# Kernel optimization log

Measured on AMD Instinct MI355X. Metric: run time of the kernel, lower is better.

The kernel has to match this reference:

```python
import jax, jax.numpy as jnp
import numpy as np
from jax import lax

B, C, H, W = 2, 3, 1024, 1024
SH, SW = 128, 128
FH, FW = H // SH, W // SW  # integer pooling factors (8, 8)
NPRE = 64
L = 0.24          # diffusion step size l
K = 0.03          # exp(log(0.03)), fixed logk for feature_extractor='none'
EPS = 1e-8
DEPS = 0.1


def _g(x):
    # g(x) = 1 / (1 + |x*x| / K^2)
    return 1.0 / (1.0 + (x * x) / (K * K))


def _conductance(feats):
    # cv: [B,1,H-1,W], ch: [B,1,H,W-1]; mean of |finite diff| over channels
    cv = _g(jnp.mean(jnp.abs(feats[:, :, 1:, :] - feats[:, :, :-1, :]), axis=1, keepdims=True))
    ch = _g(jnp.mean(jnp.abs(feats[:, :, :, 1:] - feats[:, :, :, :-1]), axis=1, keepdims=True))
    return cv, ch


def _downsample(x):
    # AdaptiveAvgPool2d((SH,SW)) with integer factor == exact mean pooling
    b = x.shape[0]
    return x.reshape(b, 1, SH, FH, SW, FW).mean(axis=(3, 5))


def _upsample(x):
    # F.interpolate(mode='nearest') with integer factor == pixel replication
    return jnp.repeat(jnp.repeat(x, FH, axis=2), FW, axis=3)


def setup_inputs() -> dict:
    key = jax.random.key(0)
    k1, k2, k3, k4 = jax.random.split(key, 4)
    guide = jax.random.normal(k1, (B, C, H, W), dtype=jnp.float32)
    y_bicubic = jax.random.uniform(k2, (B, 1, H, W), dtype=jnp.float32)
    source = jax.random.uniform(k3, (B, 1, SH, SW), dtype=jnp.float32)
    mask_lr = jax.random.uniform(k4, (B, 1, SH, SW), dtype=jnp.float32)
    return {"guide": guide, "y_bicubic": y_bicubic, "source": source, "mask_lr": mask_lr}


def _diffuse(img, guide, source, mask_inv):
    # feature_extractor == 'none': guide_feats = cat([guide, img], 1)
    feats = jnp.concatenate([guide, img], axis=1)
    cv, ch = _conductance(feats)

    def step(im, _):
        # diffuse_step: dv/dh computed from the SAME input image, then
        # vertical update applied first, horizontal second (matches torch in-place order)
        dv = im[:, :, 1:, :] - im[:, :, :-1, :]
        dh = im[:, :, :, 1:] - im[:, :, :, :-1]
        tv = L * cv * dv
        th = L * ch * dh
        im = im.at[:, :, 1:, :].add(-tv).at[:, :, :-1, :].add(tv)
        im = im.at[:, :, :, 1:].add(-th).at[:, :, :, :-1].add(th)
        # adjust_step: low-res ratio correction
        im_ss = _downsample(im)
        ratio_ss = jnp.where(mask_inv, 1.0, source / (im_ss + EPS))
        return im * _upsample(ratio_ss), None

    img, _ = lax.scan(step, img, None, length=NPRE)
    return img, cv, ch


def reference(guide, y_bicubic, source, mask_lr):
    # shift depths if min(source) <= deps (jit-safe scalar select)
    shift = jnp.where(jnp.min(source) <= DEPS, DEPS, 0.0).astype(source.dtype)
    source = source + shift
    img = y_bicubic + shift
    mask_inv = mask_lr < 0.5
    y_pred, cv, ch = _diffuse(img, guide, source, mask_inv)
    y_pred = y_pred - shift
    return y_pred, cv, ch
```

## Files before the change

kernel.cpp:

```cpp
#include <hip/hip_runtime.h>


#define BB 2
#define HH 1024
#define WW 1024
#define NPIX (HH * WW)
#define CVN (1023 * 1024)
#define SHW (128 * 128)
#define LL 0.24f
#define KK2 (0.03f * 0.03f)
#define EPSF 1e-8f
#define DEPSF 0.1f
#define NPRE 64
#define NB 512
#define TPB 256

typedef unsigned long long u64;
typedef unsigned int uint4v __attribute__((ext_vector_type(4)));
#define ROWPAR ((size_t)NB * 2 * 128)
#define COLPAR ((size_t)NB * 2 * 32)

__device__ inline void ust4(void* p, uint4v q) {
    asm volatile("global_store_dwordx4 %0, %1, off sc0 sc1" :: "v"(p), "v"(q) : "memory");
}
__device__ inline uint4v uld4(const void* p) {
    uint4v r;
    asm volatile("global_load_dwordx4 %0, %1, off sc0 sc1" : "=v"(r) : "v"(p) : "memory");
    return r;
}
__device__ inline void vwait() { asm volatile("s_waitcnt vmcnt(0)" ::: "memory"); }

__device__ inline void pub2(u64* p, float v0, float v1, unsigned s) {
    uint4v q;
    q.x = __float_as_uint(v0); q.y = s;
    q.z = __float_as_uint(v1); q.w = s;
    ust4(p, q);
}
__device__ inline bool tags_ok(uint4v a, uint4v b, unsigned s) {
    return a.y == s && a.w == s && b.y == s && b.w == s;
}
__device__ inline float4 vals_of(uint4v a, uint4v b) {
    return make_float4(__uint_as_float(a.x), __uint_as_float(a.z),
                       __uint_as_float(b.x), __uint_as_float(b.z));
}

__device__ inline float gfun(float d) { return 1.0f / (1.0f + (d * d) / KK2); }

#define BAR() do { asm volatile("s_waitcnt lgkmcnt(0)" ::: "memory"); \
                   __builtin_amdgcn_s_barrier();                      \
                   __builtin_amdgcn_sched_barrier(0); } while (0)

__launch_bounds__(TPB, 2)
__global__ void persist_kernel(const float* __restrict__ guide, const float* __restrict__ yb,
                               const float* __restrict__ src, const float* __restrict__ mask,
                               float* __restrict__ out, float* __restrict__ out_cv,
                               float* __restrict__ out_ch,
                               u64* __restrict__ bufRow, u64* __restrict__ bufCol) {
    __shared__ float tile[2][32 * 128];
    __shared__ float sm[4];
    int blk = blockIdx.x;
    int b = blk >> 8;
    int r = blk & 255;
    int tileY = r >> 3;
    int tileX = r & 7;
    int tid = threadIdx.x;
    int cyL = tid >> 5;
    int g = tid & 31;
    int wv = tid >> 6;
    int l0 = tid & 63;
    int lx0 = g * 4;
    int ly0 = cyL * 4;
    int gx = tileX * 128 + lx0;
    int gy = tileY * 32 + ly0;

    float mmin = 1e30f;
    const float4* s4 = (const float4*)src;
    for (int i = tid; i < (BB * SHW) / 4; i += TPB) {
        float4 v = s4[i];
        mmin = fminf(mmin, fminf(fminf(v.x, v.y), fminf(v.z, v.w)));
    }
    for (int off = 32; off > 0; off >>= 1) mmin = fminf(mmin, __shfl_down(mmin, off));
    if ((tid & 63) == 0) sm[tid >> 6] = mmin;
    __syncthreads();
    float mm = fminf(fminf(sm[0], sm[1]), fminf(sm[2], sm[3]));
    float shift = (mm <= DEPSF) ? DEPSF : 0.0f;

    int ry[6];
#pragma unroll
    for (int j = 0; j < 6; ++j) {
        int y = gy - 1 + j;
        ry[j] = y < 0 ? 0 : (y > 1023 ? 1023 : y);
    }
    int cxl = (gx > 0) ? gx - 1 : 0;
    int cxr = (gx + 4 < 1024) ? gx + 4 : 1023;
    float4 z4 = make_float4(0.f, 0.f, 0.f, 0.f);
    float4 vd[5] = {z4, z4, z4, z4, z4};
    float4 hd[4] = {z4, z4, z4, z4};
    float hmd[4] = {0.f, 0.f, 0.f, 0.f};
    float4 imv[4], r0v = z4, r5v = z4;
    float slv[4], srv[4];
#pragma unroll
    for (int c = 0; c < 4; ++c) {
        const float* F = (c < 3) ? guide + ((size_t)b * 3 + c) * NPIX
                                 : yb + (size_t)b * NPIX;
        float4 rr[6];
#pragma unroll
        for (int j = 0; j < 6; ++j)
            rr[j] = *(const float4*)(F + (size_t)ry[j] * WW + gx);
#pragma unroll
        for (int j = 0; j < 5; ++j) {
            vd[j].x += fabsf(rr[j + 1].x - rr[j].x);
            vd[j].y += fabsf(rr[j + 1].y - rr[j].y);
            vd[j].z += fabsf(rr[j + 1].z - rr[j].z);
            vd[j].w += fabsf(rr[j + 1].w - rr[j].w);
        }
#pragma unroll
        for (int k = 0; k < 4; ++k) {
            float4 R = rr[k + 1];
            float sr = F[(size_t)ry[k + 1] * WW + cxr];
            float sl = F[(size_t)ry[k + 1] * WW + cxl];
            hd[k].x += fabsf(R.y - R.x);
            hd[k].y += fabsf(R.z - R.y);
            hd[k].z += fabsf(R.w - R.z);
            hd[k].w += fabsf(sr - R.w);
            hmd[k] += fabsf(R.x - sl);
            if (c == 3) { imv[k] = R; slv[k] = sl; srv[k] = sr; }
        }
        if (c == 3) { r0v = rr[0]; r5v = rr[5]; }
    }
    float4 cvR[5], chR[4];
    float hmR[4];
#pragma unroll
    for (int j = 0; j < 5; ++j) {
        int y = gy - 1 + j;
        if (y < 0 || y > 1022) {
            cvR[j] = z4;
        } else {
            cvR[j] = make_float4(gfun(vd[j].x * 0.25f), gfun(vd[j].y * 0.25f),
                                 gfun(vd[j].z * 0.25f), gfun(vd[j].w * 0.25f));
        }
    }
#pragma unroll
    for (int k = 0; k < 4; ++k) {
        chR[k] = make_float4(gfun(hd[k].x * 0.25f), gfun(hd[k].y * 0.25f),
                             gfun(hd[k].z * 0.25f), gfun(hd[k].w * 0.25f));
        if (gx + 3 == 1023) chR[k].w = 0.f;
        hmR[k] = (gx > 0) ? gfun(hmd[k] * 0.25f) : 0.f;
    }
#pragma unroll
    for (int j = 1; j < 5; ++j) {
        int y = gy + j - 1;
        if (y <= 1022)
            *(float4*)(out_cv + (size_t)b * CVN + (size_t)y * WW + gx) = cvR[j];
    }
#pragma unroll
    for (int k = 0; k < 4; ++k) {
        float* base = out_ch + (size_t)b * CVN + (size_t)(gy + k) * 1023;
        base[gx + 0] = chR[k].x;
        base[gx + 1] = chR[k].y;
        base[gx + 2] = chR[k].z;
        if (gx + 3 < 1023) base[gx + 3] = chR[k].w;
    }

    int sidx = b * SHW + (tileY * 4 + (cyL >> 1)) * 128 + tileX * 16 + (g >> 1);
    float sval = src[sidx] + shift;
    bool masked = mask[sidx] < 0.5f;

    bool upAct = (cyL == 0 && tileY > 0);
    bool dnAct = (cyL == 7 && tileY < 31);
    bool lAct  = (g == 0  && tileX > 0);
    bool rAct  = (g == 31 && tileX < 7);
    bool pubTop = (wv == 0 && tileY > 0);
    bool pubBot = (wv == 3 && tileY < 31);

    float* cur = &tile[0][0];
    float* nxt = &tile[1][0];

#pragma unroll
    for (int k = 0; k < 4; ++k) {
        float4 v = imv[k];
        v.x += shift; v.y += shift; v.z += shift; v.w += shift;
        *(float4*)&cur[(ly0 + k) * 128 + lx0] = v;
    }
    float4 hUp = z4, hDn = z4;
    float xlR[4] = {0.f, 0.f, 0.f, 0.f}, xrR[4] = {0.f, 0.f, 0.f, 0.f};
    if (upAct) { hUp = r0v; hUp.x += shift; hUp.y += shift; hUp.z += shift; hUp.w += shift; }
    if (dnAct) { hDn = r5v; hDn.x += shift; hDn.y += shift; hDn.z += shift; hDn.w += shift; }
    if (lAct) {
#pragma unroll
        for (int k = 0; k < 4; ++k) xlR[k] = slv[k] + shift;
    }
    if (rAct) {
#pragma unroll
        for (int k = 0; k < 4; ++k) xrR[k] = srv[k] + shift;
    }
    __syncthreads();

    float4 nv[4];
    for (int t = 0; t < NPRE; ++t) {
        float4 rUp = (cyL == 0) ? hUp : *(float4*)&cur[(ly0 - 1) * 128 + lx0];
        float4 rC  = *(float4*)&cur[ly0 * 128 + lx0];
        float csum = 0.f;
#pragma unroll
        for (int k = 0; k < 4; ++k) {
            float4 rDn = (k == 3 && cyL == 7) ? hDn
                       : *(float4*)&cur[(ly0 + 1 + k) * 128 + lx0];
            float4 cu = cvR[k], cd = cvR[k + 1], h4 = chR[k];
            float xl = __shfl_up(rC.w, 1);
            float xr = __shfl_down(rC.x, 1);
            float hm = hmR[k];
            if (g == 0)  xl = xlR[k];
            if (g == 31) xr = xrR[k];
            float4 a;
            a.x = rC.x + LL * (cd.x * (rDn.x - rC.x) - cu.x * (rC.x - rUp.x)
                             + h4.x * (rC.y - rC.x) - hm   * (rC.x - xl));
            a.y = rC.y + LL * (cd.y * (rDn.y - rC.y) - cu.y * (rC.y - rUp.y)
                             + h4.y * (rC.z - rC.y) - h4.x * (rC.y - rC.x));
            a.z = rC.z + LL * (cd.z * (rDn.z - rC.z) - cu.z * (rC.z - rUp.z)
                             + h4.z * (rC.w - rC.z) - h4.y * (rC.z - rC.y));
            a.w = rC.w + LL * (cd.w * (rDn.w - rC.w) - cu.w * (rC.w - rUp.w)
                             + h4.w * (xr   - rC.w) - h4.z * (rC.w - rC.z));
            nv[k] = a;
            csum += a.x + a.y + a.z + a.w;
            rUp = rC; rC = rDn;
        }
        csum += __shfl_xor(csum, 1);
        csum += __shfl_xor(csum, 32);
        float ratio = masked ? 1.0f : sval / (csum * (1.0f / 64.0f) + EPSF);

        if (t == NPRE - 1) {
            float* ob = out + (size_t)b * NPIX;
#pragma unroll
            for (int k = 0; k < 4; ++k) {
                float4 v = nv[k];
                v.x = v.x * ratio - shift; v.y = v.y * ratio - shift;
                v.z = v.z * ratio - shift; v.w = v.w * ratio - shift;
                *(float4*)(ob + (size_t)(gy + k) * WW + gx) = v;
            }
            break;
        }
#pragma unroll
        for (int k = 0; k < 4; ++k) {
            nv[k].x *= ratio; nv[k].y *= ratio; nv[k].z *= ratio; nv[k].w *= ratio;
        }

        unsigned s2 = (unsigned)(t + 1);
        size_t rOff2 = (s2 & 1) ? ROWPAR : 0;
        size_t cOff2 = (s2 & 1) ? COLPAR : 0;
        if (pubTop) {
            float a = __shfl(nv[0].x, l0 >> 1), bq = __shfl(nv[0].y, l0 >> 1);
            float c = __shfl(nv[0].z, l0 >> 1), d = __shfl(nv[0].w, l0 >> 1);
            float v0 = (l0 & 1) ? c : a, v1 = (l0 & 1) ? d : bq;
            uint4v q; q.x = __float_as_uint(v0); q.y = s2;
            q.z = __float_as_uint(v1); q.w = s2;
            ust4(&bufRow[rOff2 + ((size_t)blk * 2 + 0) * 128 + 2 * l0], q);
        }
        if (pubBot) {
            int sl = 32 + (l0 >> 1);
            float a = __shfl(nv[3].x, sl), bq = __shfl(nv[3].y, sl);
            float c = __shfl(nv[3].z, sl), d = __shfl(nv[3].w, sl);
            float v0 = (l0 & 1) ? c : a, v1 = (l0 & 1) ? d : bq;
            uint4v q; q.x = __float_as_uint(v0); q.y = s2;
            q.z = __float_as_uint(v1); q.w = s2;
            ust4(&bufRow[rOff2 + ((size_t)blk * 2 + 1) * 128 + 2 * l0], q);
        }
        if (lAct) {
            u64* p = &bufCol[cOff2 + ((size_t)blk * 2 + 0) * 32 + ly0];
            pub2(p, nv[0].x, nv[1].x, s2);
            pub2(p + 2, nv[2].x, nv[3].x, s2);
        }
        if (rAct) {
            u64* p = &bufCol[cOff2 + ((size_t)blk * 2 + 1) * 32 + ly0];
            pub2(p, nv[0].w, nv[1].w, s2);
            pub2(p + 2, nv[2].w, nv[3].w, s2);
        }

#pragma unroll
        for (int k = 0; k < 4; ++k)
            *(float4*)&nxt[(ly0 + k) * 128 + lx0] = nv[k];
        BAR();

        const u64* pUp = upAct ? &bufRow[rOff2 + (((size_t)blk - 8) * 2 + 1) * 128 + lx0] : nullptr;
        const u64* pDn = dnAct ? &bufRow[rOff2 + (((size_t)blk + 8) * 2 + 0) * 128 + lx0] : nullptr;
        const u64* pL  = lAct  ? &bufCol[cOff2 + (((size_t)blk - 1) * 2 + 1) * 32 + ly0] : nullptr;
        const u64* pR  = rAct  ? &bufCol[cOff2 + (((size_t)blk + 1) * 2 + 0) * 32 + ly0] : nullptr;
        bool needU = upAct, needD = dnAct, needL = lAct, needR = rAct;
        uint4v uA, uB, dA, dB, lA, lB, rA, rB;
        for (;;) {
            if (needU) { uA = uld4(pUp); uB = uld4(pUp + 2); }
            if (needD) { dA = uld4(pDn); dB = uld4(pDn + 2); }
            if (needL) { lA = uld4(pL);  lB = uld4(pL + 2); }
            if (needR) { rA = uld4(pR);  rB = uld4(pR + 2); }
            vwait();
            if (needU && tags_ok(uA, uB, s2)) { hUp = vals_of(uA, uB); needU = false; }
            if (needD && tags_ok(dA, dB, s2)) { hDn = vals_of(dA, dB); needD = false; }
            if (needL && tags_ok(lA, lB, s2)) {
                float4 c = vals_of(lA, lB);
                xlR[0] = c.x; xlR[1] = c.y; xlR[2] = c.z; xlR[3] = c.w;
                needL = false;
            }
            if (needR && tags_ok(rA, rB, s2)) {
                float4 c = vals_of(rA, rB);
                xrR[0] = c.x; xrR[1] = c.y; xrR[2] = c.z; xrR[3] = c.w;
                needR = false;
            }
            if (__all(!(needU || needD || needL || needR))) break;
            __builtin_amdgcn_s_sleep(1);
        }
        float* tmp = cur; cur = nxt; nxt = tmp;
    }
}

extern "C" void kernel_launch(void* const* d_in, const int* in_sizes, int n_in,
                              void* d_out, int out_size, void* d_ws, size_t ws_size,
                              hipStream_t stream) {
    const float* guide = (const float*)d_in[0];
    const float* yb    = (const float*)d_in[1];
    const float* src   = (const float*)d_in[2];
    const float* mask  = (const float*)d_in[3];

    float* out    = (float*)d_out;
    float* out_cv = out + (size_t)BB * NPIX;
    float* out_ch = out_cv + (size_t)BB * CVN;

    u64* bufRow = (u64*)d_ws;
    u64* bufCol = bufRow + 2 * ROWPAR;

    persist_kernel<<<NB, TPB, 0, stream>>>(guide, yb, src, mask, out, out_cv,
                                           out_ch, bufRow, bufCol);
}
```

Measured before the change: 254.0 us.

## Overlap halo polling with interior stencil compute in persistent diffusion loop

The halo exchange wait moves from the end of each iteration to the start of the next. Halo loads are issued first, then the interior stencil is computed with zero halos, and halo contributions are added as linear corrections once the tagged values arrive. This hides inter-block communication latency behind compute. It adds correction arithmetic and relies on the tag and sequence indexing (sP = t, parity buffers) matching what the publishers wrote.

New measurement: 231.6 us. 8.9% less time.

```diff
diff --git a/kernel.cpp b/kernel.cpp
--- a/kernel.cpp
+++ b/kernel.cpp
@@ -198,19 +198,35 @@
 
     float4 nv[4];
     for (int t = 0; t < NPRE; ++t) {
-        float4 rUp = (cyL == 0) ? hUp : *(float4*)&cur[(ly0 - 1) * 128 + lx0];
+        unsigned sP = (unsigned)t;
+        size_t rOffP = (t & 1) ? ROWPAR : 0;
+        size_t cOffP = (t & 1) ? COLPAR : 0;
+        const u64* pUp = upAct ? &bufRow[rOffP + (((size_t)blk - 8) * 2 + 1) * 128 + lx0] : nullptr;
+        const u64* pDn = dnAct ? &bufRow[rOffP + (((size_t)blk + 8) * 2 + 0) * 128 + lx0] : nullptr;
+        const u64* pL  = lAct  ? &bufCol[cOffP + (((size_t)blk - 1) * 2 + 1) * 32 + ly0] : nullptr;
+        const u64* pR  = rAct  ? &bufCol[cOffP + (((size_t)blk + 1) * 2 + 0) * 32 + ly0] : nullptr;
+        uint4v uA, uB, dA, dB, lA, lB, rA, rB;
+        bool pollRound = (t > 0);
+        if (pollRound) {
+            if (upAct) { uA = uld4(pUp); uB = uld4(pUp + 2); }
+            if (dnAct) { dA = uld4(pDn); dB = uld4(pDn + 2); }
+            if (lAct)  { lA = uld4(pL);  lB = uld4(pL + 2); }
+            if (rAct)  { rA = uld4(pR);  rB = uld4(pR + 2); }
+        }
+
+        float4 rUp = (cyL == 0) ? z4 : *(float4*)&cur[(ly0 - 1) * 128 + lx0];
         float4 rC  = *(float4*)&cur[ly0 * 128 + lx0];
         float csum = 0.f;
 #pragma unroll
         for (int k = 0; k < 4; ++k) {
-            float4 rDn = (k == 3 && cyL == 7) ? hDn
+            float4 rDn = (k == 3 && cyL == 7) ? z4
                        : *(float4*)&cur[(ly0 + 1 + k) * 128 + lx0];
             float4 cu = cvR[k], cd = cvR[k + 1], h4 = chR[k];
-            float xl = __shfl_up(rC.w, 1);
-            float xr = __shfl_down(rC.x, 1);
+            float xs = __shfl_up(rC.w, 1);
+            float xt = __shfl_down(rC.x, 1);
+            float xl = (g == 0)  ? 0.f : xs;
+            float xr = (g == 31) ? 0.f : xt;
             float hm = hmR[k];
-            if (g == 0)  xl = xlR[k];
-            if (g == 31) xr = xrR[k];
             float4 a;
             a.x = rC.x + LL * (cd.x * (rDn.x - rC.x) - cu.x * (rC.x - rUp.x)
                              + h4.x * (rC.y - rC.x) - hm   * (rC.x - xl));
@@ -224,6 +240,64 @@
             csum += a.x + a.y + a.z + a.w;
             rUp = rC; rC = rDn;
         }
+
+        if (pollRound) {
+            vwait();
+            bool needU = upAct, needD = dnAct, needL = lAct, needR = rAct;
+            for (;;) {
+                if (needU && tags_ok(uA, uB, sP)) { hUp = vals_of(uA, uB); needU = false; }
+                if (needD && tags_ok(dA, dB, sP)) { hDn = vals_of(dA, dB); needD = false; }
+                if (needL && tags_ok(lA, lB, sP)) {
+                    float4 c = vals_of(lA, lB);
+                    xlR[0] = c.x; xlR[1] = c.y; xlR[2] = c.z; xlR[3] = c.w;
+                    needL = false;
+                }
+                if (needR && tags_ok(rA, rB, sP)) {
+                    float4 c = vals_of(rA, rB);
+                    xrR[0] = c.x; xrR[1] = c.y; xrR[2] = c.z; xrR[3] = c.w;
+                    needR = false;
+                }
+                if (__all(!(needU || needD || needL || needR))) break;
+                __builtin_amdgcn_s_sleep(1);
+                if (needU) { uA = uld4(pUp); uB = uld4(pUp + 2); }
+                if (needD) { dA = uld4(pDn); dB = uld4(pDn + 2); }
+                if (needL) { lA = uld4(pL);  lB = uld4(pL + 2); }
+                if (needR) { rA = uld4(pR);  rB = uld4(pR + 2); }
+                vwait();
+            }
+        }
+
+        float cadd = 0.f;
+        if (cyL == 0) {
+            float4 cu = cvR[0];
+            float c0 = LL * cu.x * hUp.x, c1 = LL * cu.y * hUp.y;
+            float c2 = LL * cu.z * hUp.z, c3 = LL * cu.w * hUp.w;
+            nv[0].x += c0; nv[0].y += c1; nv[0].z += c2; nv[0].w += c3;
+            cadd += c0 + c1 + c2 + c3;
+        }
+        if (cyL == 7) {
+            float4 cd = cvR[4];
+            float c0 = LL * cd.x * hDn.x, c1 = LL * cd.y * hDn.y;
+            float c2 = LL * cd.z * hDn.z, c3 = LL * cd.w * hDn.w;
+            nv[3].x += c0; nv[3].y += c1; nv[3].z += c2; nv[3].w += c3;
+            cadd += c0 + c1 + c2 + c3;
+        }
+        if (g == 0) {
+#pragma unroll
+            for (int k = 0; k < 4; ++k) {
+                float c = LL * hmR[k] * xlR[k];
+                nv[k].x += c; cadd += c;
+            }
+        }
+        if (g == 31) {
+#pragma unroll
+            for (int k = 0; k < 4; ++k) {
+                float c = LL * chR[k].w * xrR[k];
+                nv[k].w += c; cadd += c;
+            }
+        }
+        csum += cadd;
+
         csum += __shfl_xor(csum, 1);
         csum += __shfl_xor(csum, 32);
         float ratio = masked ? 1.0f : sval / (csum * (1.0f / 64.0f) + EPSF);
@@ -279,34 +353,6 @@
         for (int k = 0; k < 4; ++k)
             *(float4*)&nxt[(ly0 + k) * 128 + lx0] = nv[k];
         BAR();
-
-        const u64* pUp = upAct ? &bufRow[rOff2 + (((size_t)blk - 8) * 2 + 1) * 128 + lx0] : nullptr;
-        const u64* pDn = dnAct ? &bufRow[rOff2 + (((size_t)blk + 8) * 2 + 0) * 128 + lx0] : nullptr;
-        const u64* pL  = lAct  ? &bufCol[cOff2 + (((size_t)blk - 1) * 2 + 1) * 32 + ly0] : nullptr;
-        const u64* pR  = rAct  ? &bufCol[cOff2 + (((size_t)blk + 1) * 2 + 0) * 32 + ly0] : nullptr;
-        bool needU = upAct, needD = dnAct, needL = lAct, needR = rAct;
-        uint4v uA, uB, dA, dB, lA, lB, rA, rB;
-        for (;;) {
-            if (needU) { uA = uld4(pUp); uB = uld4(pUp + 2); }
-            if (needD) { dA = uld4(pDn); dB = uld4(pDn + 2); }
-            if (needL) { lA = uld4(pL);  lB = uld4(pL + 2); }
-            if (needR) { rA = uld4(pR);  rB = uld4(pR + 2); }
-            vwait();
-            if (needU && tags_ok(uA, uB, s2)) { hUp = vals_of(uA, uB); needU = false; }
-            if (needD && tags_ok(dA, dB, s2)) { hDn = vals_of(dA, dB); needD = false; }
-            if (needL && tags_ok(lA, lB, s2)) {
-                float4 c = vals_of(lA, lB);
-                xlR[0] = c.x; xlR[1] = c.y; xlR[2] = c.z; xlR[3] = c.w;
-                needL = false;
-            }
-            if (needR && tags_ok(rA, rB, s2)) {
-                float4 c = vals_of(rA, rB);
-                xrR[0] = c.x; xrR[1] = c.y; xrR[2] = c.z; xrR[3] = c.w;
-                needR = false;
-            }
-            if (__all(!(needU || needD || needL || needR))) break;
-            __builtin_amdgcn_s_sleep(1);
-        }
         float* tmp = cur; cur = nxt; nxt = tmp;
     }
 }
```
